# Kernel tuning notes

Hardware: AMD Instinct MI355X
Metric: run time of the kernel (lower is better)

The kernel has to match this reference:

```python
import jax, jax.numpy as jnp
import numpy as np

# Dims: B=4, T=4096, D=4096, G=1, C=4, K=128, I=4 (I2=2), M=32
B, T, D = 4, 4096, 4096
G, C, K, M = 1, 4, 128, 32
I = 4  # 2*dynamic_hidden_dim
EPS = 1e-6


def setup_inputs() -> dict:
    key = jax.random.key(0)
    k1, k2, k3, k4 = jax.random.split(key, 4)
    query_vec = jax.random.normal(k1, (B, T, D), dtype=jnp.float32)
    dw1 = jax.random.normal(k2, (D, G, C, K), dtype=jnp.float32) * 0.02
    qkw = jax.random.normal(k3, (G, C, K, I, M), dtype=jnp.float32) * 0.02
    dd_w = jax.random.normal(k4, (D, G, M * C), dtype=jnp.float32) * 0.02
    return {"query_vec": query_vec, "dw1": dw1, "qkw": qkw, "dd_w": dd_w}


def _rmsnorm_noscale(x):
    var = jnp.mean(jnp.square(x), axis=-1, keepdims=True)
    return x * jax.lax.rsqrt(var + EPS)


def reference(query_vec, dw1, qkw, dd_w):
    # dw_hidden: [B,T,G,C,K]
    dw_hidden = jnp.einsum('btd,dgck->btgck', query_vec, dw1)
    dw_hidden = jax.nn.gelu(dw_hidden, approximate=False)  # torch nn.GELU() = exact erf
    # w: [B,T,G,C,I,M]; split along I into w1,w2 of [B,T,G,C,I/2,M]
    w = jnp.einsum('btgck,gckim->btgcim', dw_hidden, qkw)
    w1, w2 = jnp.split(w, 2, axis=-2)
    w1 = _rmsnorm_noscale(w1)
    # unbind along C=4: order is (pre_q, pre_k, post_q, post_k)
    pre_qw1, pre_kw1, post_qw1, post_kw1 = (w1[:, :, :, i] for i in range(4))
    pre_qw2, pre_kw2, post_qw2, post_kw2 = (w2[:, :, :, i] for i in range(4))
    # dd: [B,T,G,4M] -> tanh -> split into 4 of [B,T,G,M]
    dd = jnp.tanh(jnp.einsum('btd,dgm->btgm', query_vec, dd_w))
    pre_qdd, pre_kdd, post_qdd, post_kdd = jnp.split(dd, 4, axis=-1)
    # gen_cache=True path: KW [B,T,2,M,M]
    eye = jnp.eye(M, dtype=query_vec.dtype)
    pre_kw = jnp.einsum('bsgim,bsgin->bsmn', pre_kw1, pre_kw2) + pre_kdd[:, :, 0, :, None] * eye
    post_kw = jnp.einsum('bsgim,bsgin->bsmn', post_kw1, post_kw2) + post_kdd[:, :, 0, :, None] * eye
    KW = jnp.stack((pre_kw, post_kw), axis=-3)
    return (pre_qw1, pre_qw2, pre_kw1, pre_kw2, pre_qdd, pre_kdd,
            post_qw1, post_qw2, post_kw1, post_kw2, post_qdd, post_kdd, KW)
```

## Files before the change

### kernel.cpp

```cpp
#include <hip/hip_runtime.h>
#include <hip/hip_bf16.h>


typedef _Float16 half8 __attribute__((ext_vector_type(8)));
typedef float f32x4 __attribute__((ext_vector_type(4)));

#define BT_TOK 16384
#define DDIM   4096

static constexpr int OFF_PRE_QW1  = 0;
static constexpr int OFF_PRE_QW2  = 1048576;
static constexpr int OFF_PRE_KW1  = 2097152;
static constexpr int OFF_PRE_KW2  = 3145728;
static constexpr int OFF_PRE_QDD  = 4194304;
static constexpr int OFF_PRE_KDD  = 4718592;
static constexpr int OFF_POST_QW1 = 5242880;
static constexpr int OFF_POST_QW2 = 6291456;
static constexpr int OFF_POST_KW1 = 7340032;
static constexpr int OFF_POST_KW2 = 8388608;
static constexpr int OFF_POST_QDD = 9437184;
static constexpr int OFF_POST_KDD = 9961472;
static constexpr int OFF_KW       = 10485760;

typedef __attribute__((address_space(3))) void lds_void;
typedef const __attribute__((address_space(1))) void gbl_void;

__device__ __forceinline__ void gload16(const void* g, void* l) {
  __builtin_amdgcn_global_load_lds((gbl_void*)g, (lds_void*)l, 16, 0, 0);
}

__global__ __launch_bounds__(256) void convert_a(const float* __restrict__ q,
                                                 _Float16* __restrict__ a) {
  const int stride = gridDim.x * blockDim.x;
  for (int i = blockIdx.x * blockDim.x + threadIdx.x; i < (BT_TOK * DDIM) / 8;
       i += stride) {
    const float4* p = (const float4*)(q + (size_t)i * 8);
    float4 x = p[0], y = p[1];
    half8 h;
    h[0] = (_Float16)x.x; h[1] = (_Float16)x.y;
    h[2] = (_Float16)x.z; h[3] = (_Float16)x.w;
    h[4] = (_Float16)y.x; h[5] = (_Float16)y.y;
    h[6] = (_Float16)y.z; h[7] = (_Float16)y.w;
    *(half8*)(a + (size_t)i * 8) = h;
  }
}

__global__ __launch_bounds__(256) void build_bt(const float* __restrict__ dw1,
                                                const float* __restrict__ ddw,
                                                _Float16* __restrict__ Bt) {
  __shared__ float tile[64][65];
  const int bn = blockIdx.x % 10, bd = blockIdx.x / 10;
  const int n0 = bn * 64, d0 = bd * 64;
  const int tid = threadIdx.x;
  const int ln = tid & 63;
  const int rr = tid >> 6;
#pragma unroll
  for (int i = 0; i < 16; ++i) {
    int dl = rr + i * 4;
    int d = d0 + dl, n = n0 + ln;
    float v = (n < 512) ? dw1[d * 512 + n] : ddw[d * 128 + (n - 512)];
    tile[dl][ln] = v;
  }
  __syncthreads();
#pragma unroll
  for (int i = 0; i < 16; ++i) {
    int nl = rr + i * 4;
    Bt[(size_t)(n0 + nl) * DDIM + d0 + ln] = (_Float16)tile[ln][nl];
  }
}

__global__ __launch_bounds__(256) void build_qkwT(const float* __restrict__ qkw,
                                                  _Float16* __restrict__ qT) {
  const int c = blockIdx.x;
  for (int e = threadIdx.x; e < 16384; e += 256) {
    int n = e >> 7, k = e & 127;
    qT[c * 16384 + n * 128 + k] = (_Float16)qkw[c * 16384 + k * 128 + n];
  }
}

__global__ __launch_bounds__(256) void gemm_main(const _Float16* __restrict__ A,
                                                 const _Float16* __restrict__ Bt,
                                                 _Float16* __restrict__ Hg,
                                                 float* __restrict__ out) {
  __shared__ _Float16 As[8192];
  __shared__ _Float16 Bs[8192];

  int wg = (int)blockIdx.x;
  wg = (wg & 7) * 80 + (wg >> 3);
  const int mtile = wg / 5, ntile = wg - mtile * 5;
  const int m0 = mtile << 7, n0 = ntile << 7;

  const int tid = threadIdx.x;
  const int wave = tid >> 6, lane = tid & 63;
  const int lq = lane >> 4, lc = lane & 15;

  int aoff[4], boff[4];
  _Float16* lA[4];
  _Float16* lB[4];
#pragma unroll
  for (int j = 0; j < 4; ++j) {
    int slot = j * 256 + wave * 64 + lane;
    int row = slot >> 3;
    int gs = (slot & 7) ^ (row & 7);
    aoff[j] = (m0 + row) * DDIM + gs * 8;
    boff[j] = (n0 + row) * DDIM + gs * 8;
    lA[j] = As + j * 2048 + wave * 512;
    lB[j] = Bs + j * 2048 + wave * 512;
  }
  const int wm = (wave >> 1) << 6, wn = (wave & 1) << 6;

  f32x4 acc[4][4];
#pragma unroll
  for (int i = 0; i < 4; ++i)
#pragma unroll
    for (int j = 0; j < 4; ++j) acc[i][j] = f32x4{0.f, 0.f, 0.f, 0.f};

  for (int k0 = 0; k0 < DDIM; k0 += 64) {
#pragma unroll
    for (int j = 0; j < 4; ++j) gload16(A + aoff[j] + k0, lA[j]);
#pragma unroll
    for (int j = 0; j < 4; ++j) gload16(Bt + boff[j] + k0, lB[j]);
    __syncthreads();
#pragma unroll
    for (int kk = 0; kk < 2; ++kk) {
      half8 af[4], bf[4];
      const int kb = kk * 4 + lq;
#pragma unroll
      for (int f = 0; f < 4; ++f) {
        int rowA = wm + f * 16 + lc;
        af[f] = *(const half8*)(As + rowA * 64 + ((kb ^ (rowA & 7)) << 3));
        int rowB = wn + f * 16 + lc;
        bf[f] = *(const half8*)(Bs + rowB * 64 + ((kb ^ (rowB & 7)) << 3));
      }
#pragma unroll
      for (int mf = 0; mf < 4; ++mf)
#pragma unroll
        for (int nf = 0; nf < 4; ++nf)
          acc[mf][nf] = __builtin_amdgcn_mfma_f32_16x16x32_f16(
              af[mf], bf[nf], acc[mf][nf], 0, 0, 0);
    }
    __syncthreads();
  }

  if (ntile < 4) {
#pragma unroll
    for (int mf = 0; mf < 4; ++mf)
#pragma unroll
      for (int nf = 0; nf < 4; ++nf)
#pragma unroll
        for (int r = 0; r < 4; ++r) {
          int row = m0 + wm + mf * 16 + lq * 4 + r;
          int col = n0 + wn + nf * 16 + lc;
          float v = acc[mf][nf][r];
          float g = 0.5f * v * (1.0f + erff(v * 0.70710678118654752f));
          Hg[(size_t)row * 512 + col] = (_Float16)g;
        }
  } else {
#pragma unroll
    for (int mf = 0; mf < 4; ++mf)
#pragma unroll
      for (int nf = 0; nf < 4; ++nf)
#pragma unroll
        for (int r = 0; r < 4; ++r) {
          int row = m0 + wm + mf * 16 + lq * 4 + r;
          int j = wn + nf * 16 + lc;
          int t = j >> 5;
          int base = (t & 2) ? ((t & 1) ? OFF_POST_KDD : OFF_POST_QDD)
                             : ((t & 1) ? OFF_PRE_KDD : OFF_PRE_QDD);
          out[base + row * 32 + (j & 31)] = tanhf(acc[mf][nf][r]);
        }
  }
}

__global__ __launch_bounds__(256) void epilogue_k(const _Float16* __restrict__ Hg,
                                                  const _Float16* __restrict__ qT,
                                                  float* __restrict__ out) {
  __shared__ float stash[2][4][16][32];
  __shared__ float ddl[2][16][32];
  const int tid = threadIdx.x;
  const int wave = tid >> 6, lane = tid & 63;
  const int lq = lane >> 4, lc = lane & 15;
  const int tok0 = blockIdx.x * 16;
  const int c = wave;

#pragma unroll
  for (int z = 0; z < 4; ++z) {
    int idx = z * 256 + tid;
    int pp = idx >> 9, tl = (idx >> 5) & 15, m = idx & 31;
    ddl[pp][tl][m] =
        out[(pp ? OFF_POST_KDD : OFF_PRE_KDD) + (tok0 + tl) * 32 + m];
  }

  const _Float16* arow = Hg + (size_t)(tok0 + lc) * 512 + c * 128 + lq * 8;
  half8 af[4];
#pragma unroll
  for (int kf = 0; kf < 4; ++kf) af[kf] = *(const half8*)(arow + kf * 32);

  f32x4 acc[8];
#pragma unroll
  for (int nf = 0; nf < 8; ++nf) acc[nf] = f32x4{0.f, 0.f, 0.f, 0.f};
#pragma unroll
  for (int nf = 0; nf < 8; ++nf) {
    const _Float16* brow = qT + c * 16384 + (nf * 16 + lc) * 128 + lq * 8;
#pragma unroll
    for (int kf = 0; kf < 4; ++kf) {
      half8 bf = *(const half8*)(brow + kf * 32);
      acc[nf] = __builtin_amdgcn_mfma_f32_16x16x32_f16(af[kf], bf, acc[nf], 0, 0, 0);
    }
  }

  const int w1base = (c >> 1) * OFF_POST_QW1 + (c & 1) * OFF_PRE_KW1;
  const int w2base = w1base + OFF_PRE_QW2;
  const int cs = c >> 1;
  const bool isk = (c & 1);

#pragma unroll
  for (int i = 0; i < 4; ++i) {
    float vn0[4], vn1[4];
#pragma unroll
    for (int r = 0; r < 4; ++r) {
      vn0[r] = acc[2 * i][r];
      vn1[r] = acc[2 * i + 1][r];
    }
    if (i < 2) {
#pragma unroll
      for (int r = 0; r < 4; ++r) {
        float ss = vn0[r] * vn0[r] + vn1[r] * vn1[r];
        ss += __shfl_xor(ss, 1);
        ss += __shfl_xor(ss, 2);
        ss += __shfl_xor(ss, 4);
        ss += __shfl_xor(ss, 8);
        float sc = rsqrtf(ss * 0.03125f + 1e-6f);
        vn0[r] *= sc;
        vn1[r] *= sc;
      }
    }
    const int basei = ((i < 2) ? w1base : w2base) + (i & 1) * 32;
#pragma unroll
    for (int r = 0; r < 4; ++r) {
      int token = tok0 + lq * 4 + r;
      out[basei + token * 64 + lc] = vn0[r];
      out[basei + token * 64 + 16 + lc] = vn1[r];
      if (isk) {
        stash[cs][i][lq * 4 + r][lc] = vn0[r];
        stash[cs][i][lq * 4 + r][16 + lc] = vn1[r];
      }
    }
  }
  __syncthreads();

#pragma unroll 8
  for (int it = 0; it < 128; ++it) {
    int flat = it * 256 + tid;
    int pp = flat >> 14, rest = flat & 16383;
    int tl = rest >> 10, mrow = (rest >> 5) & 31, n = rest & 31;
    float v = stash[pp][0][tl][mrow] * stash[pp][2][tl][n] +
              stash[pp][1][tl][mrow] * stash[pp][3][tl][n];
    if (mrow == n) v += ddl[pp][tl][n];
    out[OFF_KW + (tok0 + tl) * 2048 + pp * 1024 + mrow * 32 + n] = v;
  }
}

extern "C" void kernel_launch(void* const* d_in, const int* in_sizes, int n_in,
                              void* d_out, int out_size, void* d_ws, size_t ws_size,
                              hipStream_t stream) {
  const float* q   = (const float*)d_in[0];
  const float* dw1 = (const float*)d_in[1];
  const float* qkw = (const float*)d_in[2];
  const float* ddw = (const float*)d_in[3];
  float* out = (float*)d_out;

  _Float16* Ah = (_Float16*)d_ws;
  _Float16* Bt = Ah + (size_t)BT_TOK * DDIM;
  _Float16* Hg = Bt + (size_t)640 * DDIM;
  _Float16* qT = Hg + (size_t)BT_TOK * 512;

  convert_a<<<2048, 256, 0, stream>>>(q, Ah);
  build_bt<<<640, 256, 0, stream>>>(dw1, ddw, Bt);
  build_qkwT<<<4, 256, 0, stream>>>(qkw, qT);
  gemm_main<<<640, 256, 0, stream>>>(Ah, Bt, Hg, out);
  epilogue_k<<<1024, 256, 0, stream>>>(Hg, qT, out);
}
```

Before: 654.7 us.

## Double-buffer GEMM LDS tiles and stage transposes and epilogue rows through shared memory

The main GEMM now keeps two LDS buffers for A and B, so the global-to-LDS load for the next K step is issued before the MFMA work on the current step, and one barrier per iteration is dropped. The qkw transpose kernel now reads rows coalesced into a padded shared tile and writes the transposed output coalesced. The epilogue kernel loads each token block's Hg rows into LDS with coalesced 16-byte loads before the MFMA fragment reads. The cost is double the LDS footprint in the GEMM, which can lower occupancy, plus an extra barrier in the epilogue.

```diff
diff --git a/kernel.cpp b/kernel.cpp
--- a/kernel.cpp
+++ b/kernel.cpp
@@ -71,10 +71,17 @@
 
 __global__ __launch_bounds__(256) void build_qkwT(const float* __restrict__ qkw,
                                                   _Float16* __restrict__ qT) {
+  __shared__ float t[128][129];
   const int c = blockIdx.x;
-  for (int e = threadIdx.x; e < 16384; e += 256) {
-    int n = e >> 7, k = e & 127;
-    qT[c * 16384 + n * 128 + k] = (_Float16)qkw[c * 16384 + k * 128 + n];
+  const float* src = qkw + c * 16384;
+  for (int z = threadIdx.x; z < 16384; z += 256) {
+    int k = z >> 7, n = z & 127;
+    t[k][n] = src[z];
+  }
+  __syncthreads();
+  for (int z = threadIdx.x; z < 16384; z += 256) {
+    int n = z >> 7, k = z & 127;
+    qT[c * 16384 + z] = (_Float16)t[k][n];
   }
 }
 
@@ -82,8 +89,8 @@
                                                  const _Float16* __restrict__ Bt,
                                                  _Float16* __restrict__ Hg,
                                                  float* __restrict__ out) {
-  __shared__ _Float16 As[8192];
-  __shared__ _Float16 Bs[8192];
+  __shared__ _Float16 As[2][8192];
+  __shared__ _Float16 Bs[2][8192];
 
   int wg = (int)blockIdx.x;
   wg = (wg & 7) * 80 + (wg >> 3);
@@ -94,9 +101,7 @@
   const int wave = tid >> 6, lane = tid & 63;
   const int lq = lane >> 4, lc = lane & 15;
 
-  int aoff[4], boff[4];
-  _Float16* lA[4];
-  _Float16* lB[4];
+  int aoff[4], boff[4], lbase[4];
 #pragma unroll
   for (int j = 0; j < 4; ++j) {
     int slot = j * 256 + wave * 64 + lane;
@@ -104,8 +109,7 @@
     int gs = (slot & 7) ^ (row & 7);
     aoff[j] = (m0 + row) * DDIM + gs * 8;
     boff[j] = (n0 + row) * DDIM + gs * 8;
-    lA[j] = As + j * 2048 + wave * 512;
-    lB[j] = Bs + j * 2048 + wave * 512;
+    lbase[j] = j * 2048 + wave * 512;
   }
   const int wm = (wave >> 1) << 6, wn = (wave & 1) << 6;
 
@@ -115,12 +119,14 @@
 #pragma unroll
     for (int j = 0; j < 4; ++j) acc[i][j] = f32x4{0.f, 0.f, 0.f, 0.f};
 
-  for (int k0 = 0; k0 < DDIM; k0 += 64) {
-#pragma unroll
-    for (int j = 0; j < 4; ++j) gload16(A + aoff[j] + k0, lA[j]);
-#pragma unroll
-    for (int j = 0; j < 4; ++j) gload16(Bt + boff[j] + k0, lB[j]);
-    __syncthreads();
+  auto stage = [&](int b, int k0) {
+#pragma unroll
+    for (int j = 0; j < 4; ++j) gload16(A + aoff[j] + k0, &As[b][lbase[j]]);
+#pragma unroll
+    for (int j = 0; j < 4; ++j) gload16(Bt + boff[j] + k0, &Bs[b][lbase[j]]);
+  };
+
+  auto compute = [&](int b) {
 #pragma unroll
     for (int kk = 0; kk < 2; ++kk) {
       half8 af[4], bf[4];
@@ -128,9 +134,9 @@
 #pragma unroll
       for (int f = 0; f < 4; ++f) {
         int rowA = wm + f * 16 + lc;
-        af[f] = *(const half8*)(As + rowA * 64 + ((kb ^ (rowA & 7)) << 3));
+        af[f] = *(const half8*)(&As[b][rowA * 64 + ((kb ^ (rowA & 7)) << 3)]);
         int rowB = wn + f * 16 + lc;
-        bf[f] = *(const half8*)(Bs + rowB * 64 + ((kb ^ (rowB & 7)) << 3));
+        bf[f] = *(const half8*)(&Bs[b][rowB * 64 + ((kb ^ (rowB & 7)) << 3)]);
       }
 #pragma unroll
       for (int mf = 0; mf < 4; ++mf)
@@ -139,8 +145,16 @@
           acc[mf][nf] = __builtin_amdgcn_mfma_f32_16x16x32_f16(
               af[mf], bf[nf], acc[mf][nf], 0, 0, 0);
     }
+  };
+
+  stage(0, 0);
+  __syncthreads();
+  for (int t = 0; t < 63; ++t) {
+    stage((t + 1) & 1, (t + 1) << 6);
+    compute(t & 1);
     __syncthreads();
   }
+  compute(1);
 
   if (ntile < 4) {
 #pragma unroll
@@ -175,6 +189,7 @@
 __global__ __launch_bounds__(256) void epilogue_k(const _Float16* __restrict__ Hg,
                                                   const _Float16* __restrict__ qT,
                                                   float* __restrict__ out) {
+  __shared__ _Float16 hga[16][520];
   __shared__ float stash[2][4][16][32];
   __shared__ float ddl[2][16][32];
   const int tid = threadIdx.x;
@@ -185,16 +200,25 @@
 
 #pragma unroll
   for (int z = 0; z < 4; ++z) {
+    int flat = z * 256 + tid;
+    int row = flat >> 6, c16 = flat & 63;
+    *(half8*)(&hga[row][c16 * 8]) =
+        *(const half8*)(Hg + (size_t)(tok0 + row) * 512 + c16 * 8);
+  }
+
+#pragma unroll
+  for (int z = 0; z < 4; ++z) {
     int idx = z * 256 + tid;
     int pp = idx >> 9, tl = (idx >> 5) & 15, m = idx & 31;
     ddl[pp][tl][m] =
         out[(pp ? OFF_POST_KDD : OFF_PRE_KDD) + (tok0 + tl) * 32 + m];
   }
-
-  const _Float16* arow = Hg + (size_t)(tok0 + lc) * 512 + c * 128 + lq * 8;
+  __syncthreads();
+
   half8 af[4];
 #pragma unroll
-  for (int kf = 0; kf < 4; ++kf) af[kf] = *(const half8*)(arow + kf * 32);
+  for (int kf = 0; kf < 4; ++kf)
+    af[kf] = *(const half8*)(&hga[lc][c * 128 + kf * 32 + lq * 8]);
 
   f32x4 acc[8];
 #pragma unroll
```

New measurement: 667.8 us. No clear change (+2.0%).
